# Kernel optimization log

Hardware: AMD Instinct MI355X
Metric: run time of the kernel (lower is better)

The kernel has to match this reference:

```python
import jax, jax.numpy as jnp
import numpy as np

TEMPERATURE = 0.1
EPS = 1e-07


def setup_inputs() -> dict:
    key = jax.random.key(0)
    k1, k2 = jax.random.split(key)
    embeddings = jax.random.normal(k1, (4096, 768), dtype=jnp.float32)
    labels = jax.random.normal(k2, (4096, 2), dtype=jnp.float32)
    return {"embeddings": embeddings, "labels": labels}


def _supcr_dim(sims, exp_sims, lab, eps):
    # sims, exp_sims: [M, M]; lab: [M]
    M = lab.shape[0]
    dists = jnp.abs(lab[None, :] - lab[:, None])            # [M, M]
    idx = jnp.argsort(dists, axis=1)                         # row-wise sort order
    sorted_d = jnp.take_along_axis(dists, idx, axis=1)
    sorted_s = jnp.take_along_axis(exp_sims, idx, axis=1)
    # reversed cumsum (suffix sums) along each row
    suffix = jnp.flip(jnp.cumsum(jnp.flip(sorted_s, axis=1), axis=1), axis=1)
    # per-row searchsorted: first index where sorted_d >= dists[i, j]
    pos = jax.vmap(lambda sd, rd: jnp.searchsorted(sd, rd, side='left'))(sorted_d, dists)
    denom = jnp.maximum(jnp.take_along_axis(suffix, pos, axis=1), eps)
    # -log(exp(sims) / denom) == log(denom) - sims
    row_loss = jnp.log(denom) - sims
    off_diag = ~jnp.eye(M, dtype=bool)
    total = jnp.sum(jnp.where(off_diag, row_loss, 0.0))
    return total / (M * (M - 1))


def reference(embeddings, labels):
    # cosine similarity / temperature (torch F.normalize clamps norm at 1e-12)
    norm = jnp.maximum(jnp.linalg.norm(embeddings, axis=1, keepdims=True), 1e-12)
    normed = embeddings / norm
    sims = (normed @ normed.T) / TEMPERATURE                 # [M, M]
    exp_sims = jnp.exp(sims)
    # vmap over label dimensions (labels.T: [num_dims, M])
    losses = jax.vmap(lambda lab: _supcr_dim(sims, exp_sims, lab, EPS))(labels.T)
    return losses
```

## Files before the change

### kernel.cpp

```cpp
#include <hip/hip_runtime.h>
#include <hip/hip_bf16.h>
#include <math.h>

#define MM 4096
#define KK 768
#define NB64 64
#define NBK 1024
#define QSCALE 65536.0f
#define LN2 0.6931471805599453f

typedef short bf16x8 __attribute__((ext_vector_type(8)));
typedef unsigned short u16x8 __attribute__((ext_vector_type(8)));
typedef float f32x4 __attribute__((ext_vector_type(4)));

__device__ __forceinline__ float bf2f(unsigned short u) {
  return __uint_as_float(((unsigned int)u) << 16);
}
__device__ __forceinline__ unsigned short f2bf(float f) {
  __hip_bfloat16 h = __float2bfloat16(f);
  return *(unsigned short*)&h;
}

__device__ __forceinline__ void gload16(const void* g, void* l) {
#if __has_builtin(__builtin_amdgcn_global_load_lds)
  __builtin_amdgcn_global_load_lds((__attribute__((address_space(1))) void*)g,
                                   (__attribute__((address_space(3))) void*)l,
                                   16, 0, 0);
#else
  *(bf16x8*)l = *(const bf16x8*)g;
#endif
}

__global__ __launch_bounds__(256) void knorm(const float* __restrict__ emb,
                                             __hip_bfloat16* __restrict__ nb,
                                             const float* __restrict__ labels,
                                             float* __restrict__ dmm) {
  int row = blockIdx.x;
  int tid = threadIdx.x;
  if (row == MM) {
    float mn0 = 1e30f, mx0 = -1e30f, mn1 = 1e30f, mx1 = -1e30f;
    for (int q = tid; q < MM; q += 256) {
      float2 l2 = ((const float2*)labels)[q];
      mn0 = fminf(mn0, l2.x); mx0 = fmaxf(mx0, l2.x);
      mn1 = fminf(mn1, l2.y); mx1 = fmaxf(mx1, l2.y);
    }
    for (int s = 32; s; s >>= 1) {
      mn0 = fminf(mn0, __shfl_down(mn0, s, 64));
      mx0 = fmaxf(mx0, __shfl_down(mx0, s, 64));
      mn1 = fminf(mn1, __shfl_down(mn1, s, 64));
      mx1 = fmaxf(mx1, __shfl_down(mx1, s, 64));
    }
    __shared__ float redm[4][4];
    if ((tid & 63) == 0) {
      redm[0][tid >> 6] = mn0; redm[1][tid >> 6] = mx0;
      redm[2][tid >> 6] = mn1; redm[3][tid >> 6] = mx1;
    }
    __syncthreads();
    if (tid == 0) {
      dmm[0] = fminf(fminf(redm[0][0], redm[0][1]), fminf(redm[0][2], redm[0][3]));
      dmm[1] = fmaxf(fmaxf(redm[1][0], redm[1][1]), fmaxf(redm[1][2], redm[1][3]));
      dmm[2] = fminf(fminf(redm[2][0], redm[2][1]), fminf(redm[2][2], redm[2][3]));
      dmm[3] = fmaxf(fmaxf(redm[3][0], redm[3][1]), fmaxf(redm[3][2], redm[3][3]));
    }
    return;
  }
  const float* e = emb + (size_t)row * KK;
  float v0 = e[tid], v1 = e[tid + 256], v2 = e[tid + 512];
  float ss = v0 * v0 + v1 * v1 + v2 * v2;
  for (int s = 32; s; s >>= 1) ss += __shfl_down(ss, s, 64);
  __shared__ float red[4];
  if ((tid & 63) == 0) red[tid >> 6] = ss;
  __syncthreads();
  float tot = red[0] + red[1] + red[2] + red[3];
  float inv = 1.f / fmaxf(sqrtf(tot), 1e-12f);
  __hip_bfloat16* o = nb + (size_t)row * KK;
  o[tid] = __float2bfloat16(v0 * inv);
  o[tid + 256] = __float2bfloat16(v1 * inv);
  o[tid + 512] = __float2bfloat16(v2 * inv);
}

union SmemU64 {
  struct { short As[64 * 64]; short Bs[64 * 64]; } s;
  float tbuf[32][68];
};

__global__ __launch_bounds__(256) void kgemm_sym64(const __hip_bfloat16* __restrict__ A,
                                                   unsigned short* __restrict__ out,
                                                   float* __restrict__ srow) {
  __shared__ __align__(16) SmemU64 sm;
  const int tid = threadIdx.x;
  const int w = tid >> 6, l = tid & 63;
  const int wr = w >> 1, wc = w & 1;
  const int b = blockIdx.x;
  int by = (int)((129.0f - sqrtf(16641.0f - 8.0f * (float)b)) * 0.5f);
  by = min(max(by, 0), 63);
  while (by > 0 && (by * (129 - by)) / 2 > b) --by;
  while (by < 63 && (((by + 1) * (129 - (by + 1))) / 2) <= b) ++by;
  const int bx = by + (b - (by * (129 - by)) / 2);
  const int row0 = by * 64, col0 = bx * 64;
  const short* Ag = (const short*)A;

  f32x4 acc[2][2];
#pragma unroll
  for (int mi = 0; mi < 2; ++mi)
#pragma unroll
    for (int ni = 0; ni < 2; ++ni) acc[mi][ni] = (f32x4){0.f, 0.f, 0.f, 0.f};

  const int r0 = tid >> 3, s0 = tid & 7;
  const int sx = ((s0 ^ (r0 & 7)) * 8);
  const int lr = l & 15, kb = (l >> 4) * 8;
  const int xr = (lr & 7) << 3;

  for (int k0 = 0; k0 < KK; k0 += 64) {
    __syncthreads();
    gload16(Ag + (size_t)(row0 + r0) * KK + k0 + sx, &sm.s.As[tid * 8]);
    gload16(Ag + (size_t)(row0 + 32 + r0) * KK + k0 + sx, &sm.s.As[(tid + 256) * 8]);
    gload16(Ag + (size_t)(col0 + r0) * KK + k0 + sx, &sm.s.Bs[tid * 8]);
    gload16(Ag + (size_t)(col0 + 32 + r0) * KK + k0 + sx, &sm.s.Bs[(tid + 256) * 8]);
    __syncthreads();
    bf16x8 av[2][2], bv[2][2];
#pragma unroll
    for (int mi = 0; mi < 2; ++mi)
#pragma unroll
      for (int kh = 0; kh < 2; ++kh)
        av[mi][kh] = *(const bf16x8*)&sm.s.As[(wr * 32 + mi * 16 + lr) * 64 +
                                              ((kh * 32 + kb) ^ xr)];
#pragma unroll
    for (int ni = 0; ni < 2; ++ni)
#pragma unroll
      for (int kh = 0; kh < 2; ++kh)
        bv[ni][kh] = *(const bf16x8*)&sm.s.Bs[(wc * 32 + ni * 16 + lr) * 64 +
                                              ((kh * 32 + kb) ^ xr)];
#pragma unroll
    for (int kh = 0; kh < 2; ++kh)
#pragma unroll
      for (int mi = 0; mi < 2; ++mi)
#pragma unroll
        for (int ni = 0; ni < 2; ++ni)
          acc[mi][ni] = __builtin_amdgcn_mfma_f32_16x16x32_bf16(av[mi][kh], bv[ni][kh],
                                                                acc[mi][ni], 0, 0, 0);
  }

  const int quad = l >> 4;
  const bool diag = (bx == by);

#pragma unroll
  for (int mi = 0; mi < 2; ++mi) {
#pragma unroll
    for (int r = 0; r < 4; ++r) {
      const int grow = row0 + wr * 32 + mi * 16 + quad * 4 + r;
      float rsum = 0.f;
#pragma unroll
      for (int ni = 0; ni < 2; ++ni) {
        const int gcol = col0 + wc * 32 + ni * 16 + lr;
        rsum += (diag && gcol == grow) ? 0.f : acc[mi][ni][r];
      }
#pragma unroll
      for (int mask = 1; mask < 16; mask <<= 1) rsum += __shfl_xor(rsum, mask, 64);
      if (lr == 0) srow[(size_t)grow * 128 + bx * 2 + wc] = rsum / 0.1f;
    }
  }

  if (!diag) {
#pragma unroll
    for (int ni = 0; ni < 2; ++ni) {
      float csum = 0.f;
#pragma unroll
      for (int mi = 0; mi < 2; ++mi)
#pragma unroll
        for (int r = 0; r < 4; ++r) csum += acc[mi][ni][r];
      csum += __shfl_xor(csum, 16, 64);
      csum += __shfl_xor(csum, 32, 64);
      if (quad == 0)
        srow[(size_t)(col0 + wc * 32 + ni * 16 + l) * 128 + by * 2 + wr] = csum / 0.1f;
    }
  }

#pragma unroll
  for (int mi = 0; mi < 2; ++mi)
#pragma unroll
    for (int ni = 0; ni < 2; ++ni)
#pragma unroll
      for (int r = 0; r < 4; ++r)
        acc[mi][ni][r] = __expf(acc[mi][ni][r] / 0.1f);

#pragma unroll
  for (int mi = 0; mi < 2; ++mi)
#pragma unroll
    for (int r = 0; r < 4; ++r) {
      const int grow = row0 + wr * 32 + mi * 16 + quad * 4 + r;
#pragma unroll
      for (int ni = 0; ni < 2; ++ni)
        out[(size_t)grow * MM + col0 + wc * 32 + ni * 16 + lr] = f2bf(acc[mi][ni][r]);
    }

  if (!diag) {
#pragma unroll
    for (int p = 0; p < 2; ++p) {
      __syncthreads();
      if (wc == p) {
#pragma unroll
        for (int ni = 0; ni < 2; ++ni) {
          const int ltr = ni * 16 + lr;
#pragma unroll
          for (int mi = 0; mi < 2; ++mi) {
            const int cbase = wr * 32 + mi * 16 + quad * 4;
#pragma unroll
            for (int r = 0; r < 4; ++r)
              sm.tbuf[ltr][cbase + r] = acc[mi][ni][r];
          }
        }
      }
      __syncthreads();
      const int trow = tid >> 3;
      const int cseg = (tid & 7) * 8;
      const int gtr = col0 + p * 32 + trow;
      u16x8 vv;
#pragma unroll
      for (int q = 0; q < 8; ++q) vv[q] = f2bf(sm.tbuf[trow][cseg + q]);
      *(u16x8*)(out + (size_t)gtr * MM + row0 + cseg) = vv;
    }
  }
}

__global__ __launch_bounds__(256) void kgemm(const __hip_bfloat16* __restrict__ A,
                                             int rowBase,
                                             unsigned short* __restrict__ out,
                                             float* __restrict__ srow) {
  __shared__ __align__(16) short As[128 * 32];
  __shared__ __align__(16) short Bs[128 * 32];
  const int tid = threadIdx.x;
  const int w = tid >> 6, l = tid & 63;
  const int wr = w >> 1, wc = w & 1;
  const int bx = blockIdx.x;
  const int row0 = rowBase + blockIdx.y * 128;
  const int col0 = bx * 128;
  const short* Ag = (const short*)A;

  f32x4 acc[4][4];
#pragma unroll
  for (int mi = 0; mi < 4; ++mi)
#pragma unroll
    for (int ni = 0; ni < 4; ++ni) acc[mi][ni] = (f32x4){0.f, 0.f, 0.f, 0.f};

  const int r0 = tid >> 2, s0 = tid & 3;
  const int r1 = (tid + 256) >> 2;
  const int lrow = l & 15, kb = (l >> 4) * 8;

  for (int k0 = 0; k0 < KK; k0 += 32) {
    __syncthreads();
    gload16(Ag + (size_t)(row0 + r0) * KK + k0 + s0 * 8, &As[tid * 8]);
    gload16(Ag + (size_t)(row0 + r1) * KK + k0 + s0 * 8, &As[(tid + 256) * 8]);
    gload16(Ag + (size_t)(col0 + r0) * KK + k0 + s0 * 8, &Bs[tid * 8]);
    gload16(Ag + (size_t)(col0 + r1) * KK + k0 + s0 * 8, &Bs[(tid + 256) * 8]);
    __syncthreads();
    bf16x8 av[4], bv[4];
#pragma unroll
    for (int mi = 0; mi < 4; ++mi)
      av[mi] = *(const bf16x8*)&As[(wr * 64 + mi * 16 + lrow) * 32 + kb];
#pragma unroll
    for (int ni = 0; ni < 4; ++ni)
      bv[ni] = *(const bf16x8*)&Bs[(wc * 64 + ni * 16 + lrow) * 32 + kb];
#pragma unroll
    for (int mi = 0; mi < 4; ++mi)
#pragma unroll
      for (int ni = 0; ni < 4; ++ni)
        acc[mi][ni] = __builtin_amdgcn_mfma_f32_16x16x32_bf16(av[mi], bv[ni],
                                                              acc[mi][ni], 0, 0, 0);
  }

  const int quad = l >> 4;
#pragma unroll
  for (int mi = 0; mi < 4; ++mi) {
#pragma unroll
    for (int r = 0; r < 4; ++r) {
      const int grow = row0 + wr * 64 + mi * 16 + quad * 4 + r;
      float rsum = 0.f;
#pragma unroll
      for (int ni = 0; ni < 4; ++ni) {
        const int gcol = col0 + wc * 64 + ni * 16 + lrow;
        float a = acc[mi][ni][r];
        out[(size_t)(grow - rowBase) * MM + gcol] = f2bf(__expf(a / 0.1f));
        rsum += (gcol == grow) ? 0.f : a;
      }
#pragma unroll
      for (int mask = 1; mask < 16; mask <<= 1) rsum += __shfl_xor(rsum, mask, 64);
      if (lrow == 0) srow[(size_t)grow * 128 + bx * 2 + wc] = rsum / 0.1f;
    }
  }
}

__global__ __launch_bounds__(256) void kloss(const unsigned short* __restrict__ expb,
                                             int rowBase,
                                             const float* __restrict__ labels,
                                             const float* __restrict__ dmm,
                                             float* __restrict__ part_logd) {
  const int i = rowBase + blockIdx.x;
  const unsigned short* row = expb + (size_t)blockIdx.x * MM;
  __shared__ __align__(16) unsigned long long histU[2 * NBK];
  __shared__ unsigned long long wsumU[4];
  __shared__ float redf[4];
  const int tid = threadIdx.x;
  const int lane = tid & 63, wid = tid >> 6;
  const int m0 = tid * 16;
  const int b0 = tid * 8;

  const float c0 = labels[(size_t)i * 2], c1 = labels[(size_t)i * 2 + 1];
  const float tmax0 = fmaxf(fmaxf(c0 - dmm[0], dmm[1] - c0), 1e-30f);
  const float tmax1 = fmaxf(fmaxf(c1 - dmm[2], dmm[3] - c1), 1e-30f);
  const float scale0 = (float)NBK / tmax0;
  const float scale1 = (float)NBK / tmax1;

#pragma unroll
  for (int q = 0; q < 4; ++q)
    ((uint4*)histU)[tid + 256 * q] = (uint4){0, 0, 0, 0};
  __syncthreads();

  {
    u16x8 a = *(const u16x8*)(row + m0);
    u16x8 bq = *(const u16x8*)(row + m0 + 8);
    const float4* lp4 = (const float4*)(labels + (size_t)m0 * 2);
#pragma unroll
    for (int q = 0; q < 8; ++q) {
      float4 v4 = lp4[q];
      const unsigned short r0u = (2 * q < 8) ? a[2 * q] : bq[2 * q - 8];
      const unsigned short r1u = (2 * q + 1 < 8) ? a[2 * q + 1] : bq[2 * q + 1 - 8];
      const unsigned long long g0 =
          (unsigned long long)(unsigned int)(bf2f(r0u) * QSCALE + 0.5f) | (1ULL << 32);
      const unsigned long long g1 =
          (unsigned long long)(unsigned int)(bf2f(r1u) * QSCALE + 0.5f) | (1ULL << 32);
      const int a0 = min((int)(fabsf(v4.x - c0) * scale0), NBK - 1);
      const int a1 = min((int)(fabsf(v4.y - c1) * scale1), NBK - 1);
      const int b2 = min((int)(fabsf(v4.z - c0) * scale0), NBK - 1);
      const int b3 = min((int)(fabsf(v4.w - c1) * scale1), NBK - 1);
      atomicAdd(&histU[a0], g0);
      atomicAdd(&histU[NBK + a1], g0);
      atomicAdd(&histU[b2], g1);
      atomicAdd(&histU[NBK + b3], g1);
    }
  }
  __syncthreads();

  unsigned long long hh[8];
#pragma unroll
  for (int q = 0; q < 4; ++q) {
    uint4 t4 = *(const uint4*)&histU[b0 + 2 * q];
    hh[2 * q] = (unsigned long long)t4.x | ((unsigned long long)t4.y << 32);
    hh[2 * q + 1] = (unsigned long long)t4.z | ((unsigned long long)t4.w << 32);
  }
  unsigned long long S = 0;
#pragma unroll
  for (int u = 0; u < 8; ++u) S += hh[u];
  unsigned long long v = S;
#pragma unroll
  for (int s = 1; s < 64; s <<= 1) {
    unsigned long long t2 = __shfl_down(v, s, 64);
    if (lane + s < 64) v += t2;
  }
  if (lane == 0) wsumU[wid] = v;
  __syncthreads();
  unsigned long long woff = (wid == 0) ? wsumU[1] : ((wid == 2) ? wsumU[3] : 0ULL);
  unsigned long long run = woff + (v - S);

  float acc2 = 0.f;
#pragma unroll
  for (int u = 7; u >= 0; --u) {
    run += hh[u];
    const float nf = (float)(unsigned int)(hh[u] >> 32);
    const float sufq = (float)(unsigned int)run;
    acc2 += nf * __log2f(fmaxf(sufq, 1.f));
  }

  for (int s = 32; s; s >>= 1) acc2 += __shfl_down(acc2, s, 64);
  if (lane == 0) redf[wid] = acc2;
  __syncthreads();
  if (tid == 0) {
    const float tf0 = (float)(unsigned int)(wsumU[0] + wsumU[1]);
    const float tf1 = (float)(unsigned int)(wsumU[2] + wsumU[3]);
    part_logd[i] = (redf[0] + redf[1] - 65536.f - __log2f(tf0) + 16.f) * LN2;
    part_logd[MM + i] = (redf[2] + redf[3] - 65536.f - __log2f(tf1) + 16.f) * LN2;
  }
}

__global__ __launch_bounds__(256) void kred1(const float* __restrict__ part_logd,
                                             const float* __restrict__ srow,
                                             double* __restrict__ red3) {
  const int tid = threadIdx.x;
  const int base = blockIdx.x * 64;
  double ss = 0.0, s0 = 0.0, s1 = 0.0;
  for (int q = tid; q < 64 * 128; q += 256)
    ss += (double)srow[(size_t)base * 128 + q];
  if (tid < 64) {
    s0 = (double)part_logd[base + tid];
    s1 = (double)part_logd[MM + base + tid];
  }
  for (int s = 32; s; s >>= 1) {
    s0 += __shfl_down(s0, s, 64);
    s1 += __shfl_down(s1, s, 64);
    ss += __shfl_down(ss, s, 64);
  }
  __shared__ double red[3][4];
  if ((tid & 63) == 0) {
    red[0][tid >> 6] = s0; red[1][tid >> 6] = s1; red[2][tid >> 6] = ss;
  }
  __syncthreads();
  if (tid == 0) {
    red3[blockIdx.x * 3 + 0] = red[0][0] + red[0][1] + red[0][2] + red[0][3];
    red3[blockIdx.x * 3 + 1] = red[1][0] + red[1][1] + red[1][2] + red[1][3];
    red3[blockIdx.x * 3 + 2] = red[2][0] + red[2][1] + red[2][2] + red[2][3];
  }
}

__global__ __launch_bounds__(64) void kred2(const double* __restrict__ red3,
                                            float* __restrict__ out) {
  const int t = threadIdx.x;
  double s0 = red3[t * 3 + 0], s1 = red3[t * 3 + 1], ss = red3[t * 3 + 2];
  for (int s = 32; s; s >>= 1) {
    s0 += __shfl_down(s0, s, 64);
    s1 += __shfl_down(s1, s, 64);
    ss += __shfl_down(ss, s, 64);
  }
  if (t == 0) {
    const double n = (double)MM * (double)(MM - 1);
    out[0] = (float)((s0 - ss) / n);
    out[1] = (float)((s1 - ss) / n);
  }
}

extern "C" void kernel_launch(void* const* d_in, const int* in_sizes, int n_in,
                              void* d_out, int out_size, void* d_ws, size_t ws_size,
                              hipStream_t stream) {
  const float* emb = (const float*)d_in[0];
  const float* labels = (const float*)d_in[1];
  float* out = (float*)d_out;
  char* ws = (char*)d_ws;

  size_t off = 0;
  auto alloc = [&](size_t bytes) {
    void* p = ws + off;
    off = (off + bytes + 255) & ~(size_t)255;
    return p;
  };
  __hip_bfloat16* nb = (__hip_bfloat16*)alloc((size_t)MM * KK * 2);
  float* dmm = (float*)alloc(4 * 4);
  float* part_logd = (float*)alloc((size_t)2 * MM * 4);
  float* srow = (float*)alloc((size_t)MM * 128 * 4);
  double* red3 = (double*)alloc((size_t)64 * 3 * 8);
  size_t fixed = off;

  size_t avail = (ws_size > fixed) ? (ws_size - fixed) : 0;
  long long cr = (long long)(avail / ((size_t)MM * 2));
  cr = (cr / 128) * 128;
  if (cr > MM) cr = MM;
  if (cr < 128) cr = 128;
  int chunk_rows = (int)cr;
  unsigned short* expb = (unsigned short*)(ws + fixed);

  knorm<<<MM + 1, 256, 0, stream>>>(emb, nb, labels, dmm);

  if (chunk_rows == MM) {
    kgemm_sym64<<<NB64 * (NB64 + 1) / 2, 256, 0, stream>>>(nb, expb, srow);
    kloss<<<MM, 256, 0, stream>>>(expb, 0, labels, dmm, part_logd);
  } else {
    hipMemsetAsync(srow, 0, (size_t)MM * 128 * 4, stream);
    for (int base = 0; base < MM; base += chunk_rows) {
      int rows = MM - base < chunk_rows ? MM - base : chunk_rows;
      kgemm<<<dim3(MM / 128, rows / 128), 256, 0, stream>>>(nb, base, expb, srow);
      kloss<<<rows, 256, 0, stream>>>(expb, base, labels, dmm, part_logd);
    }
  }
  kred1<<<64, 256, 0, stream>>>(part_logd, srow, red3);
  kred2<<<1, 64, 0, stream>>>(red3, out);
}
```

Baseline: 77.93 us.

## Widen GEMM K-tile, vectorize row normalization, fold row-sum reduction into loss

```diff
diff --git a/kernel.cpp b/kernel.cpp
--- a/kernel.cpp
+++ b/kernel.cpp
@@ -35,9 +35,8 @@
                                              __hip_bfloat16* __restrict__ nb,
                                              const float* __restrict__ labels,
                                              float* __restrict__ dmm) {
-  int row = blockIdx.x;
-  int tid = threadIdx.x;
-  if (row == MM) {
+  const int tid = threadIdx.x;
+  if (blockIdx.x == MM / 4) {
     float mn0 = 1e30f, mx0 = -1e30f, mn1 = 1e30f, mx1 = -1e30f;
     for (int q = tid; q < MM; q += 256) {
       float2 l2 = ((const float2*)labels)[q];
@@ -64,23 +63,27 @@
     }
     return;
   }
-  const float* e = emb + (size_t)row * KK;
-  float v0 = e[tid], v1 = e[tid + 256], v2 = e[tid + 512];
-  float ss = v0 * v0 + v1 * v1 + v2 * v2;
-  for (int s = 32; s; s >>= 1) ss += __shfl_down(ss, s, 64);
-  __shared__ float red[4];
-  if ((tid & 63) == 0) red[tid >> 6] = ss;
-  __syncthreads();
-  float tot = red[0] + red[1] + red[2] + red[3];
-  float inv = 1.f / fmaxf(sqrtf(tot), 1e-12f);
-  __hip_bfloat16* o = nb + (size_t)row * KK;
-  o[tid] = __float2bfloat16(v0 * inv);
-  o[tid + 256] = __float2bfloat16(v1 * inv);
-  o[tid + 512] = __float2bfloat16(v2 * inv);
+  const int w = tid >> 6, l = tid & 63;
+  const int row = blockIdx.x * 4 + w;
+  const float4* e4 = (const float4*)(emb + (size_t)row * KK);
+  float4 a = e4[l], b = e4[l + 64], c = e4[l + 128];
+  float ss = a.x * a.x + a.y * a.y + a.z * a.z + a.w * a.w +
+             b.x * b.x + b.y * b.y + b.z * b.z + b.w * b.w +
+             c.x * c.x + c.y * c.y + c.z * c.z + c.w * c.w;
+#pragma unroll
+  for (int s = 1; s < 64; s <<= 1) ss += __shfl_xor(ss, s, 64);
+  const float inv = 1.f / fmaxf(sqrtf(ss), 1e-12f);
+  unsigned short* o = (unsigned short*)(nb + (size_t)row * KK);
+  ushort4 o1 = {f2bf(a.x * inv), f2bf(a.y * inv), f2bf(a.z * inv), f2bf(a.w * inv)};
+  ushort4 o2 = {f2bf(b.x * inv), f2bf(b.y * inv), f2bf(b.z * inv), f2bf(b.w * inv)};
+  ushort4 o3 = {f2bf(c.x * inv), f2bf(c.y * inv), f2bf(c.z * inv), f2bf(c.w * inv)};
+  *(ushort4*)(o + l * 4) = o1;
+  *(ushort4*)(o + 256 + l * 4) = o2;
+  *(ushort4*)(o + 512 + l * 4) = o3;
 }
 
 union SmemU64 {
-  struct { short As[64 * 64]; short Bs[64 * 64]; } s;
+  struct { short As[64 * 128]; short Bs[64 * 128]; } s;
   float tbuf[32][68];
 };
 
@@ -106,42 +109,46 @@
 #pragma unroll
     for (int ni = 0; ni < 2; ++ni) acc[mi][ni] = (f32x4){0.f, 0.f, 0.f, 0.f};
 
-  const int r0 = tid >> 3, s0 = tid & 7;
-  const int sx = ((s0 ^ (r0 & 7)) * 8);
-  const int lr = l & 15, kb = (l >> 4) * 8;
-  const int xr = (lr & 7) << 3;
-
-  for (int k0 = 0; k0 < KK; k0 += 64) {
+  const int lr = l & 15, quad = l >> 4;
+  int srows[4], ssegs[4];
+#pragma unroll
+  for (int q = 0; q < 4; ++q) {
+    srows[q] = w * 16 + q * 4 + (l >> 4);
+    ssegs[q] = (l & 15) ^ (srows[q] & 7);
+  }
+
+  for (int k0 = 0; k0 < KK; k0 += 128) {
     __syncthreads();
-    gload16(Ag + (size_t)(row0 + r0) * KK + k0 + sx, &sm.s.As[tid * 8]);
-    gload16(Ag + (size_t)(row0 + 32 + r0) * KK + k0 + sx, &sm.s.As[(tid + 256) * 8]);
-    gload16(Ag + (size_t)(col0 + r0) * KK + k0 + sx, &sm.s.Bs[tid * 8]);
-    gload16(Ag + (size_t)(col0 + 32 + r0) * KK + k0 + sx, &sm.s.Bs[(tid + 256) * 8]);
+#pragma unroll
+    for (int q = 0; q < 4; ++q) {
+      gload16(Ag + (size_t)(row0 + srows[q]) * KK + k0 + ssegs[q] * 8,
+              &sm.s.As[(w * 16 + q * 4) * 128 + l * 8]);
+      gload16(Ag + (size_t)(col0 + srows[q]) * KK + k0 + ssegs[q] * 8,
+              &sm.s.Bs[(w * 16 + q * 4) * 128 + l * 8]);
+    }
     __syncthreads();
-    bf16x8 av[2][2], bv[2][2];
-#pragma unroll
-    for (int mi = 0; mi < 2; ++mi)
-#pragma unroll
-      for (int kh = 0; kh < 2; ++kh)
-        av[mi][kh] = *(const bf16x8*)&sm.s.As[(wr * 32 + mi * 16 + lr) * 64 +
-                                              ((kh * 32 + kb) ^ xr)];
-#pragma unroll
-    for (int ni = 0; ni < 2; ++ni)
-#pragma unroll
-      for (int kh = 0; kh < 2; ++kh)
-        bv[ni][kh] = *(const bf16x8*)&sm.s.Bs[(wc * 32 + ni * 16 + lr) * 64 +
-                                              ((kh * 32 + kb) ^ xr)];
-#pragma unroll
-    for (int kh = 0; kh < 2; ++kh)
+#pragma unroll
+    for (int kh = 0; kh < 4; ++kh) {
+      bf16x8 av[2], bv[2];
+#pragma unroll
+      for (int mi = 0; mi < 2; ++mi) {
+        const int row = wr * 32 + mi * 16 + lr;
+        av[mi] = *(const bf16x8*)&sm.s.As[row * 128 + (((kh * 4 + quad) ^ (lr & 7)) * 8)];
+      }
+#pragma unroll
+      for (int ni = 0; ni < 2; ++ni) {
+        const int row = wc * 32 + ni * 16 + lr;
+        bv[ni] = *(const bf16x8*)&sm.s.Bs[row * 128 + (((kh * 4 + quad) ^ (lr & 7)) * 8)];
+      }
 #pragma unroll
       for (int mi = 0; mi < 2; ++mi)
 #pragma unroll
         for (int ni = 0; ni < 2; ++ni)
-          acc[mi][ni] = __builtin_amdgcn_mfma_f32_16x16x32_bf16(av[mi][kh], bv[ni][kh],
+          acc[mi][ni] = __builtin_amdgcn_mfma_f32_16x16x32_bf16(av[mi], bv[ni],
                                                                 acc[mi][ni], 0, 0, 0);
-  }
-
-  const int quad = l >> 4;
+    }
+  }
+
   const bool diag = (bx == by);
 
 #pragma unroll
@@ -294,16 +301,23 @@
                                              int rowBase,
                                              const float* __restrict__ labels,
                                              const float* __restrict__ dmm,
-                                             float* __restrict__ part_logd) {
+                                             const float* __restrict__ srow,
+                                             float* __restrict__ part_logd,
+                                             float* __restrict__ part_sr) {
   const int i = rowBase + blockIdx.x;
   const unsigned short* row = expb + (size_t)blockIdx.x * MM;
   __shared__ __align__(16) unsigned long long histU[2 * NBK];
   __shared__ unsigned long long wsumU[4];
   __shared__ float redf[4];
+  __shared__ float redsr[4];
   const int tid = threadIdx.x;
   const int lane = tid & 63, wid = tid >> 6;
   const int m0 = tid * 16;
   const int b0 = tid * 8;
+
+  float sv = (tid < 128) ? srow[(size_t)i * 128 + tid] : 0.f;
+  for (int s = 32; s; s >>= 1) sv += __shfl_down(sv, s, 64);
+  if (lane == 0) redsr[wid] = sv;
 
   const float c0 = labels[(size_t)i * 2], c1 = labels[(size_t)i * 2 + 1];
   const float tmax0 = fmaxf(fmaxf(c0 - dmm[0], dmm[1] - c0), 1e-30f);
@@ -379,20 +393,20 @@
     const float tf1 = (float)(unsigned int)(wsumU[2] + wsumU[3]);
     part_logd[i] = (redf[0] + redf[1] - 65536.f - __log2f(tf0) + 16.f) * LN2;
     part_logd[MM + i] = (redf[2] + redf[3] - 65536.f - __log2f(tf1) + 16.f) * LN2;
+    part_sr[i] = redsr[0] + redsr[1];
   }
 }
 
 __global__ __launch_bounds__(256) void kred1(const float* __restrict__ part_logd,
-                                             const float* __restrict__ srow,
+                                             const float* __restrict__ part_sr,
                                              double* __restrict__ red3) {
   const int tid = threadIdx.x;
   const int base = blockIdx.x * 64;
   double ss = 0.0, s0 = 0.0, s1 = 0.0;
-  for (int q = tid; q < 64 * 128; q += 256)
-    ss += (double)srow[(size_t)base * 128 + q];
   if (tid < 64) {
     s0 = (double)part_logd[base + tid];
     s1 = (double)part_logd[MM + base + tid];
+    ss = (double)part_sr[base + tid];
   }
   for (int s = 32; s; s >>= 1) {
     s0 += __shfl_down(s0, s, 64);
@@ -444,6 +458,7 @@
   __hip_bfloat16* nb = (__hip_bfloat16*)alloc((size_t)MM * KK * 2);
   float* dmm = (float*)alloc(4 * 4);
   float* part_logd = (float*)alloc((size_t)2 * MM * 4);
+  float* part_sr = (float*)alloc((size_t)MM * 4);
   float* srow = (float*)alloc((size_t)MM * 128 * 4);
   double* red3 = (double*)alloc((size_t)64 * 3 * 8);
   size_t fixed = off;
@@ -456,19 +471,19 @@
   int chunk_rows = (int)cr;
   unsigned short* expb = (unsigned short*)(ws + fixed);
 
-  knorm<<<MM + 1, 256, 0, stream>>>(emb, nb, labels, dmm);
+  knorm<<<MM / 4 + 1, 256, 0, stream>>>(emb, nb, labels, dmm);
 
   if (chunk_rows == MM) {
     kgemm_sym64<<<NB64 * (NB64 + 1) / 2, 256, 0, stream>>>(nb, expb, srow);
-    kloss<<<MM, 256, 0, stream>>>(expb, 0, labels, dmm, part_logd);
+    kloss<<<MM, 256, 0, stream>>>(expb, 0, labels, dmm, srow, part_logd, part_sr);
   } else {
     hipMemsetAsync(srow, 0, (size_t)MM * 128 * 4, stream);
     for (int base = 0; base < MM; base += chunk_rows) {
       int rows = MM - base < chunk_rows ? MM - base : chunk_rows;
       kgemm<<<dim3(MM / 128, rows / 128), 256, 0, stream>>>(nb, base, expb, srow);
-      kloss<<<rows, 256, 0, stream>>>(expb, base, labels, dmm, part_logd);
-    }
-  }
-  kred1<<<64, 256, 0, stream>>>(part_logd, srow, red3);
+      kloss<<<rows, 256, 0, stream>>>(expb, base, labels, dmm, srow, part_logd, part_sr);
+    }
+  }
+  kred1<<<64, 256, 0, stream>>>(part_logd, part_sr, red3);
   kred2<<<1, 64, 0, stream>>>(red3, out);
 }
```

After: 78.21 us. Within noise of the previous version (+0.4%).
